# Kernel tuning notes

Hardware: AMD Instinct MI355X
Metric: run time of the kernel (lower is better)

## Reference

```python
import math
import jax, jax.numpy as jnp
import numpy as np

B, L, H, E = 2, 4096, 8, 64          # q/k/v input layout [B, L, H, E], H*E = embed_dim = 512
NUM_HEADS = 4                        # num_heads // 2
HEAD_DIM = 64                        # embed_dim // NUM_HEADS // 2
LAMBDA_INIT = 0.8 - 0.6 * math.exp(-0.3 * 0)  # depth = 0 -> 0.2


def setup_inputs() -> dict:
    key = jax.random.key(0)
    ks = jax.random.split(key, 8)
    q = jax.random.normal(ks[0], (B, L, H, E), jnp.float32)
    k = jax.random.normal(ks[1], (B, L, H, E), jnp.float32)
    v = jax.random.normal(ks[2], (B, L, H, E), jnp.float32)
    attn_mask = jnp.zeros((L, L), jnp.float32)
    lambda_q1 = 0.1 * jax.random.normal(ks[3], (HEAD_DIM,), jnp.float32)
    lambda_k1 = 0.1 * jax.random.normal(ks[4], (HEAD_DIM,), jnp.float32)
    lambda_q2 = 0.1 * jax.random.normal(ks[5], (HEAD_DIM,), jnp.float32)
    lambda_k2 = 0.1 * jax.random.normal(ks[6], (HEAD_DIM,), jnp.float32)
    return {"q": q, "k": k, "v": v, "attn_mask": attn_mask,
            "lambda_q1": lambda_q1, "lambda_k1": lambda_k1,
            "lambda_q2": lambda_q2, "lambda_k2": lambda_k2}


def reference(q, k, v, attn_mask, lambda_q1, lambda_k1, lambda_q2, lambda_k2):
    Bq, Lq, Hq, Eq = q.shape
    scaling = HEAD_DIM ** (-0.5)
    # split each attention head into two differential sub-heads
    qh = q.reshape(Bq, Lq, 2 * NUM_HEADS, HEAD_DIM).transpose(0, 2, 1, 3) * scaling  # [B,2h,L,d]
    kh = k.reshape(Bq, Lq, 2 * NUM_HEADS, HEAD_DIM).transpose(0, 2, 1, 3)            # [B,2h,L,d]
    vh = v.reshape(Bq, Lq, NUM_HEADS, 2 * HEAD_DIM).transpose(0, 2, 1, 3)            # [B,h,L,2d]

    scores = jnp.einsum('bhld,bhsd->bhls', qh, kh)  # [B,2h,L,L]
    scores = jnp.nan_to_num(scores) + attn_mask
    probs = jax.nn.softmax(scores, axis=-1)

    lam1 = jnp.exp(jnp.sum(lambda_q1 * lambda_k1))
    lam2 = jnp.exp(jnp.sum(lambda_q2 * lambda_k2))
    lam_full = lam1 - lam2 + LAMBDA_INIT

    probs = probs.reshape(Bq, NUM_HEADS, 2, Lq, Lq)
    w = probs[:, :, 0] - lam_full * probs[:, :, 1]          # [B,h,L,L]
    out = jnp.einsum('bhls,bhsd->bhld', w, vh)              # [B,h,L,2d]
    out = out * (1.0 - LAMBDA_INIT)
    return out.transpose(0, 2, 1, 3).reshape(Bq, Lq, Hq, Eq)
```

## Files before the change

### kernel.cpp

```cpp
#include <hip/hip_runtime.h>
#include <hip/hip_bf16.h>


typedef __attribute__((ext_vector_type(8))) short s16x8;
typedef __attribute__((ext_vector_type(16))) float f32x16;
typedef __attribute__((ext_vector_type(4))) unsigned int u32x4;

#define MFMA32(a,b,c) __builtin_amdgcn_mfma_f32_32x32x16_bf16(a,b,c,0,0,0)
#define GLD16(gp, lp) __builtin_amdgcn_global_load_lds( \
    (__attribute__((address_space(1))) void*)(gp), \
    (__attribute__((address_space(3))) void*)(lp), 16, 0, 0)

__device__ __forceinline__ unsigned pk2(float a, float b){
  union { __hip_bfloat162 h; unsigned u; } cv;
  cv.h = __float22bfloat162_rn(float2{a, b});
  return cv.u;
}

__global__ void k_prep_qk(const float* __restrict__ q, const float* __restrict__ k,
                          char* __restrict__ qfr, char* __restrict__ kfr){
  int idx = blockIdx.x*256 + threadIdx.x;
  int j8 = idx & 7;
  int l  = (idx >> 3) & 4095;
  int h  = (idx >> 15) & 7;
  int b  = idx >> 18;
  size_t src = ((size_t)(b*4096 + l))*512 + h*64 + j8*8;
  const float* qp = q + src;
  const float* kp = k + src;
  const float s = 0.125f * 1.4426950408889634f;
  u32x4 qw, kw;
  #pragma unroll
  for (int i=0;i<4;i++){
    qw[i] = pk2(qp[2*i]*s, qp[2*i+1]*s);
    kw[i] = pk2(kp[2*i],   kp[2*i+1]);
  }
  int dstep = j8 >> 1, hi = j8 & 1;
  int lane16 = (l & 31) + 32*hi;
  size_t qdst = ((((size_t)(b*8+h)*128 + (l>>5))*4 + dstep) << 10) + (size_t)lane16*16;
  size_t kdst = ((((size_t)(b*8+h)*64 + (l>>6))*8 + ((l>>5)&1)*4 + dstep) << 10) + (size_t)lane16*16;
  *(u32x4*)(qfr + qdst) = qw;
  *(u32x4*)(kfr + kdst) = kw;
}

__global__ void k_prep_v(const float* __restrict__ v, char* __restrict__ vfr,
                         const float* __restrict__ lq1, const float* __restrict__ lk1,
                         const float* __restrict__ lq2, const float* __restrict__ lk2,
                         float* __restrict__ lam_out){
  if (blockIdx.x == 0 && threadIdx.x < 64){
    int l = threadIdx.x;
    float p1 = lq1[l]*lk1[l];
    float p2 = lq2[l]*lk2[l];
    #pragma unroll
    for (int m=1;m<64;m<<=1){ p1 += __shfl_xor(p1,m,64); p2 += __shfl_xor(p2,m,64); }
    if (l==0) lam_out[0] = expf(p1) - expf(p2) + 0.2f;
  }
  __shared__ float tl[64][132];
  int bid = blockIdx.x;
  int tile = bid & 63, hp = (bid>>6)&3, b = bid>>8;
  int t = threadIdx.x;
  #pragma unroll
  for (int i=0;i<32;i++){
    int idx = t + i*256;
    int s = idx >> 7, e = idx & 127;
    tl[s][e] = v[((size_t)(b*4096 + tile*64 + s))*512 + hp*128 + e];
  }
  __syncthreads();
  size_t base = ((size_t)((b*4+hp)*64 + tile))*16384;
  #pragma unroll
  for (int i=0;i<4;i++){
    int idx = t + i*256;
    int g = idx >> 6, l = idx & 63;
    int eb = g >> 2, ss = g & 3;
    int e = eb*32 + (l & 31);
    int s0 = ss*16 + (l>>5)*8;
    u32x4 w;
    #pragma unroll
    for (int jj=0;jj<4;jj++) w[jj] = pk2(tl[s0+2*jj][e], tl[s0+2*jj+1][e]);
    *(u32x4*)(vfr + base + g*1024 + l*16) = w;
  }
}

__device__ __forceinline__ void swap32(unsigned a, unsigned bv, int lane,
                                       unsigned &r0, unsigned &r1){
#if __has_builtin(__builtin_amdgcn_permlane32_swap)
  auto pr = __builtin_amdgcn_permlane32_swap(a, bv, false, false);
  r0 = pr[0]; r1 = pr[1];
#else
  unsigned ax = (unsigned)__shfl_xor((int)a, 32, 64);
  unsigned bx = (unsigned)__shfl_xor((int)bv, 32, 64);
  bool lo = lane < 32;
  r0 = lo ? a  : bx;
  r1 = lo ? ax : bv;
#endif
}
__device__ __forceinline__ s16x8 mkfrag2(const f32x16& p, int base, int lane){
  unsigned A0 = pk2(p[base+0],p[base+1]), A1 = pk2(p[base+2],p[base+3]);
  unsigned B0 = pk2(p[base+4],p[base+5]), B1 = pk2(p[base+6],p[base+7]);
  unsigned w0,w1,w2,w3;
  swap32(A0,B0,lane,w0,w2);
  swap32(A1,B1,lane,w1,w3);
  union { unsigned u[4]; s16x8 v; } r;
  r.u[0]=w0; r.u[1]=w1; r.u[2]=w2; r.u[3]=w3;
  return r.v;
}

__launch_bounds__(256, 2)
__global__ void k_attn(const char* __restrict__ qfrag, const char* __restrict__ kfrag,
                       const char* __restrict__ vfrag, const float* __restrict__ lamp,
                       float* __restrict__ out){
  __shared__ __align__(16) char lds[34048];
  int tid = threadIdx.x, lane = tid & 63, wave = tid >> 6;
  int bid = blockIdx.x;
  int y = bid & 7, qt = bid >> 3;
  int b = y >> 2, hp = y & 3;
  int sh = wave & 1, qh = wave >> 1;
  int lq = lane & 31, hi = lane >> 5;

  s16x8 qf[4];
  {
    const char* qp = qfrag + ((((size_t)(b*8 + 2*hp + sh)*128 + (qt*2 + qh))*4) << 10);
    #pragma unroll
    for (int d=0; d<4; d++) qf[d] = *(const s16x8*)(qp + d*1024 + lane*16);
  }
  const f32x16 Z = {0.f,0.f,0.f,0.f,0.f,0.f,0.f,0.f,0.f,0.f,0.f,0.f,0.f,0.f,0.f,0.f};
  f32x16 o[4];
  #pragma unroll
  for (int eb=0; eb<4; eb++) o[eb] = Z;
  float den = 0.f;

  const char* gKsh = kfrag + ((size_t)(b*8 + 2*hp + sh))*64*8192;
  const char* gV   = vfrag + ((size_t)(b*4 + hp))*64*16384;
  const char* sgV  = gV + wave*4096;
  int vld = wave*4096;

#define STAGE_V(SLOT, TT) { const char* src_ = sgV + (size_t)(TT)*16384 + lane*16; \
    char* dst_ = (char*)lds + (SLOT)*16384 + vld; \
    _Pragma("unroll") \
    for (int i_=0;i_<4;i_++) GLD16(src_ + i_*1024, dst_ + i_*1024); }

#define KLOAD(KR, TT) { const char* ksrc_ = gKsh + (size_t)(TT)*8192 + lane*16; \
    _Pragma("unroll") \
    for (int i_=0;i_<8;i_++) KR[i_] = *(const s16x8*)(ksrc_ + i_*1024); }

#define QKPAIR(KR, SA, SB) { \
    __builtin_amdgcn_s_setprio(1); \
    SA = MFMA32(KR[0], qf[0], Z); \
    SB = MFMA32(KR[4], qf[0], Z); \
    __builtin_amdgcn_s_setprio(0); \
    _Pragma("unroll") \
    for (int d=1; d<4; d++){ \
      __builtin_amdgcn_s_setprio(1); \
      SA = MFMA32(KR[d],   qf[d], SA); \
      SB = MFMA32(KR[4+d], qf[d], SB); \
      __builtin_amdgcn_s_setprio(0); \
    } }

#define SOFTMX(SA, SB) { \
    _Pragma("unroll") \
    for (int i=0;i<16;i++){ \
      SA[i] = __builtin_amdgcn_exp2f(SA[i]); \
      SB[i] = __builtin_amdgcn_exp2f(SB[i]); \
    } \
    float c0 = SA[0]+SB[0], c1 = SA[1]+SB[1], c2 = SA[2]+SB[2], c3 = SA[3]+SB[3]; \
    _Pragma("unroll") \
    for (int i=4; i<16; i+=4){ \
      c0 += SA[i]   + SB[i]; \
      c1 += SA[i+1] + SB[i+1]; \
      c2 += SA[i+2] + SB[i+2]; \
      c3 += SA[i+3] + SB[i+3]; \
    } \
    den += (c0+c1) + (c2+c3); \
    pf[0] = mkfrag2(SA, 0, lane); \
    pf[1] = mkfrag2(SA, 8, lane); \
    pf[2] = mkfrag2(SB, 0, lane); \
    pf[3] = mkfrag2(SB, 8, lane); }

#define PVSTEP(VS) { const char* Vb_ = lds + (VS)*16384; \
    _Pragma("unroll") \
    for (int ss=0; ss<4; ss++){ \
      _Pragma("unroll") \
      for (int eb=0; eb<4; eb++){ \
        s16x8 vf_ = *(const s16x8*)(Vb_ + (eb*4+ss)*1024 + lane*16); \
        __builtin_amdgcn_s_setprio(1); \
        o[eb] = MFMA32(vf_, pf[ss], o[eb]); \
        __builtin_amdgcn_s_setprio(0); \
      } } }

#define BODY(T, KRL, KRQ, VSW, VSR, SCA, SCB, SNA, SNB, LDK, STGV, DOQK) { \
    if (LDK)  KLOAD(KRL, (T)+2) \
    if (STGV) STAGE_V(VSW, (T)+1) \
    if (DOQK) QKPAIR(KRQ, SNA, SNB) \
    SOFTMX(SCA, SCB) \
    PVSTEP(VSR) \
    if ((T) < 63) __syncthreads(); }

  s16x8 pf[4];
  s16x8 kA[8], kB[8];
  f32x16 sA0, sB0, sA1, sB1;

  KLOAD(kA, 0)
  KLOAD(kB, 1)
  STAGE_V(0, 0)
  __syncthreads();
  QKPAIR(kA, sA0, sB0)

  for (int j=0; j<62; j+=2){
    BODY(j,   kA, kB, 1, 0, sA0, sB0, sA1, sB1, 1, 1, 1)
    BODY(j+1, kB, kA, 0, 1, sA1, sB1, sA0, sB0, 1, 1, 1)
  }
  BODY(62, kA, kB, 1, 0, sA0, sB0, sA1, sB1, 0, 1, 1)
  BODY(63, kB, kA, 0, 1, sA1, sB1, sA0, sB0, 0, 0, 0)

  den += __shfl_xor(den, 32, 64);

  __syncthreads();
  float invl = 1.0f / den;
  float lam = lamp[0];
  float* xb = (float*)lds;
  if (sh){
    float sc1 = lam * invl;
    float* dst = xb + qh*4224 + lq*132;
    #pragma unroll
    for (int eb=0;eb<4;eb++){
      #pragma unroll
      for (int tq=0;tq<4;tq++){
        int e = eb*32 + 8*tq + 4*hi;
        float4 w;
        w.x = o[eb][4*tq+0]*sc1; w.y = o[eb][4*tq+1]*sc1;
        w.z = o[eb][4*tq+2]*sc1; w.w = o[eb][4*tq+3]*sc1;
        *(float4*)(dst + e) = w;
      }
    }
  }
  __syncthreads();
  if (!sh){
    const float* srcp = xb + qh*4224 + lq*132;
    int qrow = qt*64 + qh*32 + lq;
    float* op = out + ((size_t)(b*4096 + qrow))*512 + hp*128;
    #pragma unroll
    for (int eb=0;eb<4;eb++){
      #pragma unroll
      for (int tq=0;tq<4;tq++){
        int e = eb*32 + 8*tq + 4*hi;
        float4 w1 = *(const float4*)(srcp + e);
        float4 r;
        r.x = 0.8f*(o[eb][4*tq+0]*invl - w1.x);
        r.y = 0.8f*(o[eb][4*tq+1]*invl - w1.y);
        r.z = 0.8f*(o[eb][4*tq+2]*invl - w1.z);
        r.w = 0.8f*(o[eb][4*tq+3]*invl - w1.w);
        *(float4*)(op + e) = r;
      }
    }
  }
#undef STAGE_V
#undef KLOAD
#undef QKPAIR
#undef SOFTMX
#undef PVSTEP
#undef BODY
}

extern "C" void kernel_launch(void* const* d_in, const int* in_sizes, int n_in,
                              void* d_out, int out_size, void* d_ws, size_t ws_size,
                              hipStream_t stream){
  const float* q   = (const float*)d_in[0];
  const float* k   = (const float*)d_in[1];
  const float* v   = (const float*)d_in[2];
  const float* lq1 = (const float*)d_in[4];
  const float* lk1 = (const float*)d_in[5];
  const float* lq2 = (const float*)d_in[6];
  const float* lk2 = (const float*)d_in[7];
  float* out = (float*)d_out;

  char* ws = (char*)d_ws;
  char* qfr = ws;
  char* kfr = ws + 8388608;
  char* vfr = ws + 16777216;
  float* lam = (float*)(ws + 25165824);

  k_prep_qk<<<2048, 256, 0, stream>>>(q, k, qfr, kfr);
  k_prep_v <<<512,  256, 0, stream>>>(v, vfr, lq1, lk1, lq2, lk2, lam);
  k_attn   <<<512,  256, 0, stream>>>(qfr, kfr, vfr, lam, out);
}
```

Measured before the change: 131.9 us.

## Merge QK and V prep kernels and coarsen MFMA priority regions

Fuses the two preprocessing kernels into one launch of 2560 blocks, with blocks below 2048 converting Q/K and the rest transposing V and computing lambda. This drops one kernel launch and its tail. It also moves the s_setprio raise and lower to wrap each whole MFMA chain rather than each pair of MFMAs. The K fragment loads are unrolled by hand with a second base pointer. The fused kernel now reserves the V transpose's shared-memory tile for every block, including Q/K blocks that never use it, which may reduce occupancy for those blocks.

```diff
diff --git a/kernel.cpp b/kernel.cpp
--- a/kernel.cpp
+++ b/kernel.cpp
@@ -17,36 +17,41 @@
   return cv.u;
 }
 
-__global__ void k_prep_qk(const float* __restrict__ q, const float* __restrict__ k,
-                          char* __restrict__ qfr, char* __restrict__ kfr){
-  int idx = blockIdx.x*256 + threadIdx.x;
-  int j8 = idx & 7;
-  int l  = (idx >> 3) & 4095;
-  int h  = (idx >> 15) & 7;
-  int b  = idx >> 18;
-  size_t src = ((size_t)(b*4096 + l))*512 + h*64 + j8*8;
-  const float* qp = q + src;
-  const float* kp = k + src;
-  const float s = 0.125f * 1.4426950408889634f;
-  u32x4 qw, kw;
-  #pragma unroll
-  for (int i=0;i<4;i++){
-    qw[i] = pk2(qp[2*i]*s, qp[2*i+1]*s);
-    kw[i] = pk2(kp[2*i],   kp[2*i+1]);
-  }
-  int dstep = j8 >> 1, hi = j8 & 1;
-  int lane16 = (l & 31) + 32*hi;
-  size_t qdst = ((((size_t)(b*8+h)*128 + (l>>5))*4 + dstep) << 10) + (size_t)lane16*16;
-  size_t kdst = ((((size_t)(b*8+h)*64 + (l>>6))*8 + ((l>>5)&1)*4 + dstep) << 10) + (size_t)lane16*16;
-  *(u32x4*)(qfr + qdst) = qw;
-  *(u32x4*)(kfr + kdst) = kw;
-}
-
-__global__ void k_prep_v(const float* __restrict__ v, char* __restrict__ vfr,
-                         const float* __restrict__ lq1, const float* __restrict__ lk1,
-                         const float* __restrict__ lq2, const float* __restrict__ lk2,
-                         float* __restrict__ lam_out){
-  if (blockIdx.x == 0 && threadIdx.x < 64){
+__global__ void k_prep(const float* __restrict__ q, const float* __restrict__ k,
+                       const float* __restrict__ v,
+                       char* __restrict__ qfr, char* __restrict__ kfr,
+                       char* __restrict__ vfr,
+                       const float* __restrict__ lq1, const float* __restrict__ lk1,
+                       const float* __restrict__ lq2, const float* __restrict__ lk2,
+                       float* __restrict__ lam_out){
+  __shared__ float tl[64][132];
+  int bid = blockIdx.x;
+  if (bid < 2048){
+    int idx = bid*256 + threadIdx.x;
+    int j8 = idx & 7;
+    int l  = (idx >> 3) & 4095;
+    int h  = (idx >> 15) & 7;
+    int b  = idx >> 18;
+    size_t src = ((size_t)(b*4096 + l))*512 + h*64 + j8*8;
+    const float* qp = q + src;
+    const float* kp = k + src;
+    const float s = 0.125f * 1.4426950408889634f;
+    u32x4 qw, kw;
+    #pragma unroll
+    for (int i=0;i<4;i++){
+      qw[i] = pk2(qp[2*i]*s, qp[2*i+1]*s);
+      kw[i] = pk2(kp[2*i],   kp[2*i+1]);
+    }
+    int dstep = j8 >> 1, hi = j8 & 1;
+    int lane16 = (l & 31) + 32*hi;
+    size_t qdst = ((((size_t)(b*8+h)*128 + (l>>5))*4 + dstep) << 10) + (size_t)lane16*16;
+    size_t kdst = ((((size_t)(b*8+h)*64 + (l>>6))*8 + ((l>>5)&1)*4 + dstep) << 10) + (size_t)lane16*16;
+    *(u32x4*)(qfr + qdst) = qw;
+    *(u32x4*)(kfr + kdst) = kw;
+    return;
+  }
+  int vbid = bid - 2048;
+  if (vbid == 0 && threadIdx.x < 64){
     int l = threadIdx.x;
     float p1 = lq1[l]*lk1[l];
     float p2 = lq2[l]*lk2[l];
@@ -54,9 +59,7 @@
     for (int m=1;m<64;m<<=1){ p1 += __shfl_xor(p1,m,64); p2 += __shfl_xor(p2,m,64); }
     if (l==0) lam_out[0] = expf(p1) - expf(p2) + 0.2f;
   }
-  __shared__ float tl[64][132];
-  int bid = blockIdx.x;
-  int tile = bid & 63, hp = (bid>>6)&3, b = bid>>8;
+  int tile = vbid & 63, hp = (vbid>>6)&3, b = vbid>>8;
   int t = threadIdx.x;
   #pragma unroll
   for (int i=0;i<32;i++){
@@ -138,22 +141,24 @@
     _Pragma("unroll") \
     for (int i_=0;i_<4;i_++) GLD16(src_ + i_*1024, dst_ + i_*1024); }
 
-#define KLOAD(KR, TT) { const char* ksrc_ = gKsh + (size_t)(TT)*8192 + lane*16; \
-    _Pragma("unroll") \
-    for (int i_=0;i_<8;i_++) KR[i_] = *(const s16x8*)(ksrc_ + i_*1024); }
+#define KLOAD(KR, TT) { \
+    const char* k0_ = gKsh + (size_t)(TT)*8192 + lane*16; \
+    const char* k1_ = k0_ + 4096; \
+    KR[0] = *(const s16x8*)(k0_);        KR[1] = *(const s16x8*)(k0_ + 1024); \
+    KR[2] = *(const s16x8*)(k0_ + 2048); KR[3] = *(const s16x8*)(k0_ + 3072); \
+    KR[4] = *(const s16x8*)(k1_);        KR[5] = *(const s16x8*)(k1_ + 1024); \
+    KR[6] = *(const s16x8*)(k1_ + 2048); KR[7] = *(const s16x8*)(k1_ + 3072); }
 
 #define QKPAIR(KR, SA, SB) { \
     __builtin_amdgcn_s_setprio(1); \
     SA = MFMA32(KR[0], qf[0], Z); \
     SB = MFMA32(KR[4], qf[0], Z); \
-    __builtin_amdgcn_s_setprio(0); \
     _Pragma("unroll") \
     for (int d=1; d<4; d++){ \
-      __builtin_amdgcn_s_setprio(1); \
       SA = MFMA32(KR[d],   qf[d], SA); \
       SB = MFMA32(KR[4+d], qf[d], SB); \
-      __builtin_amdgcn_s_setprio(0); \
-    } }
+    } \
+    __builtin_amdgcn_s_setprio(0); }
 
 #define SOFTMX(SA, SB) { \
     _Pragma("unroll") \
@@ -176,15 +181,15 @@
     pf[3] = mkfrag2(SB, 8, lane); }
 
 #define PVSTEP(VS) { const char* Vb_ = lds + (VS)*16384; \
+    __builtin_amdgcn_s_setprio(1); \
     _Pragma("unroll") \
     for (int ss=0; ss<4; ss++){ \
       _Pragma("unroll") \
       for (int eb=0; eb<4; eb++){ \
         s16x8 vf_ = *(const s16x8*)(Vb_ + (eb*4+ss)*1024 + lane*16); \
-        __builtin_amdgcn_s_setprio(1); \
         o[eb] = MFMA32(vf_, pf[ss], o[eb]); \
-        __builtin_amdgcn_s_setprio(0); \
-      } } }
+      } } \
+    __builtin_amdgcn_s_setprio(0); }
 
 #define BODY(T, KRL, KRQ, VSW, VSR, SCA, SCB, SNA, SNB, LDK, STGV, DOQK) { \
     if (LDK)  KLOAD(KRL, (T)+2) \
@@ -278,7 +283,6 @@
   char* vfr = ws + 16777216;
   float* lam = (float*)(ws + 25165824);
 
-  k_prep_qk<<<2048, 256, 0, stream>>>(q, k, qfr, kfr);
-  k_prep_v <<<512,  256, 0, stream>>>(v, vfr, lq1, lk1, lq2, lk2, lam);
-  k_attn   <<<512,  256, 0, stream>>>(qfr, kfr, vfr, lam, out);
-}
+  k_prep<<<2560, 256, 0, stream>>>(q, k, v, qfr, kfr, vfr, lq1, lk1, lq2, lk2, lam);
+  k_attn<<<512,  256, 0, stream>>>(qfr, kfr, vfr, lam, out);
+}
```

Result: no change. 132.8 us (+0.7%).
